# Kernel optimization log

Measured on AMD Instinct MI355X. Metric: run time of the kernel, lower is better.

## Reference

```python
import jax, jax.numpy as jnp
import numpy as np

DIM = 512
CODEBOOK_SIZE = 8192
B, N = 8, 2048
EPS = 1e-12


def setup_inputs() -> dict:
    key = jax.random.key(0)
    k1, k2, k3 = jax.random.split(key, 3)
    x = jax.random.normal(k1, (B, N, DIM), dtype=jnp.float32)
    # matches torch.randn(codebook_size, dim) * dim ** -0.5
    codebook = jax.random.normal(k2, (CODEBOOK_SIZE, DIM), dtype=jnp.float32) * DIM ** -0.5
    # nn.Linear(dim, dim, bias=False) weight, applied as x @ W.T
    W = jax.random.normal(k3, (DIM, DIM), dtype=jnp.float32) * DIM ** -0.5
    return {"x": x, "codebook": codebook, "W": W}


def _l2norm(t):
    return t / jnp.maximum(jnp.linalg.norm(t, axis=-1, keepdims=True), EPS)


def _rotate_from_to(q, x):
    """Rotation trick: forward value == q, gradient flows through x via a
    detached Householder-style rotation (R = I - 2ww^T + 2 q_hat x_hat^T)
    and detached norm rescaling."""
    sg = jax.lax.stop_gradient
    norm_x = jnp.linalg.norm(x, axis=-1, keepdims=True)
    norm_q = jnp.linalg.norm(q, axis=-1, keepdims=True)
    x_hat = x / jnp.maximum(norm_x, EPS)
    q_hat = q / jnp.maximum(norm_q, EPS)
    w = sg(_l2norm(x_hat + q_hat))
    x_hat_d, q_hat_d = sg(x_hat), sg(q_hat)
    e = x
    rotated = (e
               - 2.0 * jnp.sum(e * w, axis=-1, keepdims=True) * w
               + 2.0 * jnp.sum(e * x_hat_d, axis=-1, keepdims=True) * q_hat_d)
    return rotated * sg(norm_q / jnp.maximum(norm_x, EPS))


def reference(x, codebook, W):
    # implicit codebook = Linear(codebook)
    codes = jnp.einsum('cd,ed->ce', codebook, W)  # [C, d]
    d2 = -2.0 * jnp.einsum('bnd,cd->bnc', x, codes) + jnp.sum(codes * codes, axis=-1)
    indices = jnp.argmin(jax.lax.stop_gradient(d2), axis=-1)  # [b, n] int
    quantized = codes[indices]  # gather -> [b, n, d]
    commit_loss = jnp.mean((jax.lax.stop_gradient(x) - quantized) ** 2)
    quantized = _rotate_from_to(quantized, x)
    return quantized, indices, commit_loss
```

## Files before the change

kernel.cpp:

```cpp
#include <hip/hip_runtime.h>


#define DIMK  512
#define CBN   8192
#define MROWS 16384

#define SX 24.0f
#define SC 500.0f
#define INV_SS (1.0f / (SX * SC))
#define DKEY  1231
#define NSLOT 3

#define WS_CODES   0UL
#define WS_XQ      16777216UL
#define WS_CQ      25165824UL
#define WS_NORMS   29360128UL
#define WS_CAND    29392896UL
#define WS_CBH     29392896UL
#define WS_CBL     37781504UL
#define WS_WH      54558720UL
#define WS_WL      55083008UL
#define WS_LOSSP   55607296UL

typedef short s16x8 __attribute__((ext_vector_type(8)));
typedef int   i32x4 __attribute__((ext_vector_type(4)));
typedef float f32x4 __attribute__((ext_vector_type(4)));

__device__ __forceinline__ unsigned short f2bf(float f) {
    unsigned u = __float_as_uint(f);
    unsigned r = u + 0x7FFFu + ((u >> 16) & 1u);
    return (unsigned short)(r >> 16);
}
__device__ __forceinline__ float bf2f(unsigned short h) {
    return __uint_as_float(((unsigned)h) << 16);
}
__device__ __forceinline__ void load_lds16(const void* g, void* l) {
    __builtin_amdgcn_global_load_lds((const __attribute__((address_space(1))) void*)g,
                                     (__attribute__((address_space(3))) void*)l,
                                     16, 0, 0);
}
__device__ __forceinline__ signed char q8(float v, float s) {
    return (signed char)__float2int_rn(fminf(fmaxf(v * s, -127.0f), 127.0f));
}

__global__ __launch_bounds__(256) void prep(
        const float* __restrict__ x, const float* __restrict__ cb, const float* __restrict__ W,
        signed char* __restrict__ xq,
        unsigned short* __restrict__ cbh, unsigned short* __restrict__ cbl,
        unsigned short* __restrict__ wh, unsigned short* __restrict__ wl,
        float* __restrict__ norms) {
    const int b = blockIdx.x;
    const int t = threadIdx.x;
    if (b < 8192) {
        const int i = b * 256 + t;
        float4 v = ((const float4*)x)[i];
        char4 c;
        c.x = q8(v.x, SX); c.y = q8(v.y, SX); c.z = q8(v.z, SX); c.w = q8(v.w, SX);
        ((char4*)xq)[i] = c;
    } else if (b < 12288) {
        const int i = (b - 8192) * 256 + t;
        float4 v = ((const float4*)cb)[i];
        ushort4 h, l;
        h.x = f2bf(v.x); l.x = f2bf(v.x - bf2f(h.x));
        h.y = f2bf(v.y); l.y = f2bf(v.y - bf2f(h.y));
        h.z = f2bf(v.z); l.z = f2bf(v.z - bf2f(h.z));
        h.w = f2bf(v.w); l.w = f2bf(v.w - bf2f(h.w));
        ((ushort4*)cbh)[i] = h;
        ((ushort4*)cbl)[i] = l;
    } else if (b < 12544) {
        const int i = (b - 12288) * 256 + t;
        float4 v = ((const float4*)W)[i];
        ushort4 h, l;
        h.x = f2bf(v.x); l.x = f2bf(v.x - bf2f(h.x));
        h.y = f2bf(v.y); l.y = f2bf(v.y - bf2f(h.y));
        h.z = f2bf(v.z); l.z = f2bf(v.z - bf2f(h.z));
        h.w = f2bf(v.w); l.w = f2bf(v.w - bf2f(h.w));
        ((ushort4*)wh)[i] = h;
        ((ushort4*)wl)[i] = l;
    } else {
        const int i = (b - 12544) * 256 + t;
        norms[i] = 0.0f;
    }
}

__global__ __launch_bounds__(512) void codes_mfma(
        const unsigned short* __restrict__ Ah_g, const unsigned short* __restrict__ Al_g,
        const unsigned short* __restrict__ Bh_g, const unsigned short* __restrict__ Bl_g,
        float* __restrict__ C, signed char* __restrict__ Cq, float* __restrict__ Norms) {
    __shared__ __align__(16) unsigned short Ahi[2][128 * 32];
    __shared__ __align__(16) unsigned short Alo[2][128 * 32];
    __shared__ __align__(16) unsigned short Bhi[2][128 * 32];
    __shared__ __align__(16) unsigned short Blo[2][128 * 32];

    const int t    = threadIdx.x;
    const int w    = t >> 6;
    const int lane = t & 63;
    const int quad = lane >> 4;
    const int l16  = lane & 15;
    const int wm   = w & 3, wn = w >> 2;
    const int rowBase = blockIdx.x * 128;
    const int colBase = blockIdx.y * 128;

    f32x4 acc[2][4];
    #pragma unroll
    for (int i = 0; i < 2; ++i)
        #pragma unroll
        for (int j = 0; j < 4; ++j)
            acc[i][j] = (f32x4)(0.0f);

    const int mr = t >> 2;
    const int kq = ((t & 3) ^ ((t >> 3) & 3)) * 8;
    const size_t gxa = (size_t)(rowBase + mr) * DIMK + kq;
    const size_t gca = (size_t)(colBase + mr) * DIMK + kq;
    const int l0 = w * 512;

    const int swz8 = (quad ^ ((l16 >> 1) & 3)) * 8;

#define CODES_STAGE(NXT, K0)                                   \
    do {                                                       \
        load_lds16(Ah_g + gxa + (K0), &Ahi[NXT][l0]);          \
        load_lds16(Al_g + gxa + (K0), &Alo[NXT][l0]);          \
        load_lds16(Bh_g + gca + (K0), &Bhi[NXT][l0]);          \
        load_lds16(Bl_g + gca + (K0), &Blo[NXT][l0]);          \
    } while (0)

#define CODES_COMPUTE(CUR)                                                                         \
    do {                                                                                           \
        s16x8 ah[2], al[2], bh[4], bl[4];                                                          \
        _Pragma("unroll")                                                                          \
        for (int i = 0; i < 2; ++i) {                                                              \
            const int m = wm * 32 + i * 16 + l16;                                                  \
            ah[i] = *(const s16x8*)&Ahi[CUR][m * 32 + swz8];                                       \
            al[i] = *(const s16x8*)&Alo[CUR][m * 32 + swz8];                                       \
        }                                                                                          \
        _Pragma("unroll")                                                                          \
        for (int j = 0; j < 4; ++j) {                                                              \
            const int n = wn * 64 + j * 16 + l16;                                                  \
            bh[j] = *(const s16x8*)&Bhi[CUR][n * 32 + swz8];                                       \
            bl[j] = *(const s16x8*)&Blo[CUR][n * 32 + swz8];                                       \
        }                                                                                          \
        _Pragma("unroll")                                                                          \
        for (int i = 0; i < 2; ++i)                                                                \
            _Pragma("unroll")                                                                      \
            for (int j = 0; j < 4; ++j) {                                                          \
                acc[i][j] = __builtin_amdgcn_mfma_f32_16x16x32_bf16(ah[i], bh[j], acc[i][j], 0, 0, 0); \
                acc[i][j] = __builtin_amdgcn_mfma_f32_16x16x32_bf16(ah[i], bl[j], acc[i][j], 0, 0, 0); \
                acc[i][j] = __builtin_amdgcn_mfma_f32_16x16x32_bf16(al[i], bh[j], acc[i][j], 0, 0, 0); \
            }                                                                                      \
    } while (0)

    CODES_STAGE(0, 0);
    asm volatile("s_waitcnt vmcnt(0)" ::: "memory");
    __syncthreads();

    for (int k0 = 0; k0 < DIMK; k0 += 64) {
        CODES_STAGE(1, k0 + 32);
        CODES_COMPUTE(0);
        asm volatile("s_waitcnt vmcnt(0)" ::: "memory");
        __syncthreads();
        if (k0 + 64 < DIMK) {
            CODES_STAGE(0, k0 + 64);
            CODES_COMPUTE(1);
            asm volatile("s_waitcnt vmcnt(0)" ::: "memory");
            __syncthreads();
        } else {
            CODES_COMPUTE(1);
        }
    }
#undef CODES_STAGE
#undef CODES_COMPUTE

    #pragma unroll
    for (int i = 0; i < 2; ++i) {
        #pragma unroll
        for (int r = 0; r < 4; ++r) {
            const int row = rowBase + wm * 32 + i * 16 + quad * 4 + r;
            float nsum = 0.0f;
            #pragma unroll
            for (int j = 0; j < 4; ++j) {
                const int col = colBase + wn * 64 + j * 16 + l16;
                const float v = acc[i][j][r];
                C[(size_t)row * DIMK + col] = v;
                Cq[(size_t)row * DIMK + col] = q8(v, SC);
                nsum = fmaf(v, v, nsum);
            }
            nsum += __shfl_xor(nsum, 1, 64);
            nsum += __shfl_xor(nsum, 2, 64);
            nsum += __shfl_xor(nsum, 4, 64);
            nsum += __shfl_xor(nsum, 8, 64);
            if (l16 == 0) atomicAdd(&Norms[row], nsum);
        }
    }
}

__global__ __launch_bounds__(512, 6) void d2_argmin_i8(
        const signed char* __restrict__ Xq,
        const signed char* __restrict__ Cq,
        const float* __restrict__ Norms,
        unsigned* __restrict__ Cand) {
    __shared__ __align__(16) signed char Ash[2][128 * 64];
    __shared__ __align__(16) signed char Bsh[2][128 * 64];

    const int t    = threadIdx.x;
    const int w    = t >> 6;
    const int lane = t & 63;
    const int quad = lane >> 4;
    const int l16  = lane & 15;
    const int wm   = w & 3, wn = w >> 2;
    const int rowBase = blockIdx.x * 128;
    const int colBase = blockIdx.y * 128;

    i32x4 acc[2][4];
    #pragma unroll
    for (int i = 0; i < 2; ++i)
        #pragma unroll
        for (int j = 0; j < 4; ++j)
            acc[i][j] = (i32x4)(0);

    const int mr  = t >> 2;
    const int kcs = ((t & 3) ^ ((t >> 3) & 3)) * 16;
    const size_t gxa = (size_t)(rowBase + mr) * DIMK + kcs;
    const size_t gca = (size_t)(colBase + mr) * DIMK + kcs;
    const int lb = w * 1024;

    const int swz  = (quad ^ ((l16 >> 1) & 3)) * 16;
    const int aoff = (wm * 32 + l16) * 64 + swz;
    const int boff = (wn * 64 + l16) * 64 + swz;

    float nq[4];
    #pragma unroll
    for (int j = 0; j < 4; ++j)
        nq[j] = fmaf(Norms[colBase + wn * 64 + j * 16 + l16], 4096.0f, 65536.0f);

#define D2_STEP(CUR, NXT, K0, DO_STAGE, DO_SYNC)                                                   \
    do {                                                                                           \
        if (DO_STAGE) {                                                                            \
            load_lds16(Xq + gxa + (K0) + 64, &Ash[NXT][lb]);                                       \
            load_lds16(Cq + gca + (K0) + 64, &Bsh[NXT][lb]);                                       \
        }                                                                                          \
        i32x4 af0 = *(const i32x4*)&Ash[CUR][aoff];                                                \
        i32x4 af1 = *(const i32x4*)&Ash[CUR][aoff + 1024];                                         \
        __builtin_amdgcn_s_setprio(1);                                                             \
        _Pragma("unroll")                                                                          \
        for (int j = 0; j < 4; ++j) {                                                              \
            const i32x4 bfj = *(const i32x4*)&Bsh[CUR][boff + j * 1024];                           \
            acc[0][j] = __builtin_amdgcn_mfma_i32_16x16x64_i8(af0, bfj, acc[0][j], 0, 0, 0);       \
            acc[1][j] = __builtin_amdgcn_mfma_i32_16x16x64_i8(af1, bfj, acc[1][j], 0, 0, 0);       \
        }                                                                                          \
        __builtin_amdgcn_s_setprio(0);                                                             \
        if (DO_SYNC) {                                                                             \
            asm volatile("s_waitcnt vmcnt(0)" ::: "memory");                                       \
            __syncthreads();                                                                       \
        }                                                                                          \
    } while (0)

    load_lds16(Xq + gxa, &Ash[0][lb]);
    load_lds16(Cq + gca, &Bsh[0][lb]);
    asm volatile("s_waitcnt vmcnt(0)" ::: "memory");
    __syncthreads();

    D2_STEP(0, 1,   0, true,  true);
    D2_STEP(1, 0,  64, true,  true);
    D2_STEP(0, 1, 128, true,  true);
    D2_STEP(1, 0, 192, true,  true);
    D2_STEP(0, 1, 256, true,  true);
    D2_STEP(1, 0, 320, true,  true);
    D2_STEP(0, 1, 384, true,  true);
    D2_STEP(1, 0, 448, false, false);
#undef D2_STEP

    const unsigned colG = colBase + wn * 64 + l16;
    const int subtile = blockIdx.y * 2 + wn;
    const float C2 = -8192.0f * INV_SS;

    #pragma unroll
    for (int i = 0; i < 2; ++i) {
        #pragma unroll
        for (int r = 0; r < 4; ++r) {
            unsigned k[4];
            #pragma unroll
            for (int j = 0; j < 4; ++j) {
                const float kf = fmaf((float)acc[i][j][r], C2, nq[j]);
                int ki = (int)kf;
                ki = ki < 0 ? 0 : ki;
                ki = ki > 524287 ? 524287 : ki;
                k[j] = ((unsigned)ki << 13) | (colG + j * 16);
            }
            unsigned lo01 = min(k[0], k[1]), hi01 = max(k[0], k[1]);
            unsigned lo23 = min(k[2], k[3]), hi23 = max(k[2], k[3]);
            unsigned a0 = min(lo01, lo23);
            unsigned m  = max(lo01, lo23);
            unsigned tt = min(hi01, hi23);
            unsigned a1 = min(m, tt);
            unsigned a2 = max(m, tt);
            #pragma unroll
            for (int mk = 1; mk < 16; mk <<= 1) {
                const unsigned b0 = __shfl_xor(a0, mk, 64);
                const unsigned b1 = __shfl_xor(a1, mk, 64);
                const unsigned b2 = __shfl_xor(a2, mk, 64);
                const unsigned M0 = max(a0, b0);
                const unsigned m1 = min(a1, b1);
                const unsigned n0 = min(a0, b0);
                a2 = min(max(m1, M0), min(a2, b2));
                a1 = min(M0, m1);
                a0 = n0;
            }
            if (l16 == 0) {
                const int row = rowBase + wm * 32 + i * 16 + quad * 4 + r;
                unsigned* slot = Cand + ((size_t)row * 128 + subtile) * NSLOT;
                slot[0] = a0; slot[1] = a1; slot[2] = a2;
            }
        }
    }
}

__global__ __launch_bounds__(256) void refine_gather(
        const float* __restrict__ X, const float* __restrict__ Codes,
        const float* __restrict__ Norms, const unsigned* __restrict__ Cand,
        float* __restrict__ outQ, float* __restrict__ outIdx,
        float* __restrict__ lossP) {
    const int t    = threadIdx.x;
    const int w    = t >> 6;
    const int lane = t & 63;
    const int row  = blockIdx.x * 4 + w;

    const unsigned* cp = Cand + (size_t)row * 128 * NSLOT + lane * 6;
    unsigned sl[6];
    #pragma unroll
    for (int s = 0; s < 6; ++s) sl[s] = cp[s];

    unsigned mn = sl[0];
    #pragma unroll
    for (int s = 1; s < 6; ++s) mn = min(mn, sl[s]);
    #pragma unroll
    for (int mask = 1; mask < 64; mask <<= 1)
        mn = min(mn, (unsigned)__shfl((int)mn, lane ^ mask, 64));
    const unsigned thrp = (((mn >> 13) + DKEY) << 13) | 0x1FFFu;

    const float4 xa = *(const float4*)(X + (size_t)row * DIMK + lane * 8);
    const float4 xb = *(const float4*)(X + (size_t)row * DIMK + lane * 8 + 4);

    float bestD = __builtin_inff();
    unsigned bestIdx = 0xFFFFFFFFu;

    #pragma unroll
    for (int s = 0; s < 6; ++s) {
        unsigned long long bm = __ballot(sl[s] <= thrp);
        while (bm) {
            const int src = __ffsll(bm) - 1;
            bm &= bm - 1;
            const unsigned sv = (unsigned)__shfl((int)sl[s], src, 64);
            const unsigned idx = sv & 0x1FFFu;
            const float4 ca = *(const float4*)(Codes + (size_t)idx * DIMK + lane * 8);
            const float4 cbv = *(const float4*)(Codes + (size_t)idx * DIMK + lane * 8 + 4);
            float s2 = xa.x * ca.x + xa.y * ca.y + xa.z * ca.z + xa.w * ca.w
                     + xb.x * cbv.x + xb.y * cbv.y + xb.z * cbv.z + xb.w * cbv.w;
            #pragma unroll
            for (int mm = 1; mm < 64; mm <<= 1) s2 += __shfl_xor(s2, mm, 64);
            const float d2 = fmaf(-2.0f, s2, Norms[idx]);
            if (d2 < bestD || (d2 == bestD && idx < bestIdx)) { bestD = d2; bestIdx = idx; }
        }
    }

    const float4 qa = *(const float4*)(Codes + (size_t)bestIdx * DIMK + lane * 8);
    const float4 qb = *(const float4*)(Codes + (size_t)bestIdx * DIMK + lane * 8 + 4);
    *(float4*)(outQ + (size_t)row * DIMK + lane * 8) = qa;
    *(float4*)(outQ + (size_t)row * DIMK + lane * 8 + 4) = qb;
    float dx0 = xa.x - qa.x, dx1 = xa.y - qa.y, dx2 = xa.z - qa.z, dx3 = xa.w - qa.w;
    float dy0 = xb.x - qb.x, dy1 = xb.y - qb.y, dy2 = xb.z - qb.z, dy3 = xb.w - qb.w;
    float s = dx0 * dx0 + dx1 * dx1 + dx2 * dx2 + dx3 * dx3
            + dy0 * dy0 + dy1 * dy1 + dy2 * dy2 + dy3 * dy3;
    #pragma unroll
    for (int off = 32; off > 0; off >>= 1) s += __shfl_down(s, off);
    if (lane == 0) {
        lossP[row] = s;
        outIdx[row] = (float)bestIdx;
    }
}

__global__ __launch_bounds__(1024) void finalize_loss(const float* __restrict__ lossPartials,
                                                      float* __restrict__ outLoss) {
    const int t = threadIdx.x;
    const float4* p = (const float4*)lossPartials;
    const float4 a = p[t];
    const float4 b = p[t + 1024];
    const float4 c = p[t + 2048];
    const float4 d = p[t + 3072];
    float s = (a.x + a.y + a.z + a.w) + (b.x + b.y + b.z + b.w)
            + (c.x + c.y + c.z + c.w) + (d.x + d.y + d.z + d.w);
    #pragma unroll
    for (int off = 32; off > 0; off >>= 1) s += __shfl_down(s, off);
    __shared__ float red[16];
    if ((t & 63) == 0) red[t >> 6] = s;
    __syncthreads();
    if (t < 64) {
        float v = (t < 16) ? red[t] : 0.0f;
        v += __shfl_down(v, 8, 64);
        v += __shfl_down(v, 4, 64);
        v += __shfl_down(v, 2, 64);
        v += __shfl_down(v, 1, 64);
        if (t == 0)
            *outLoss = v * (1.0f / (float)((size_t)MROWS * DIMK));
    }
}

extern "C" void kernel_launch(void* const* d_in, const int* in_sizes, int n_in,
                              void* d_out, int out_size, void* d_ws, size_t ws_size,
                              hipStream_t stream) {
    const float* x  = (const float*)d_in[0];
    const float* cb = (const float*)d_in[1];
    const float* W  = (const float*)d_in[2];
    float* out = (float*)d_out;

    char* ws = (char*)d_ws;
    float* codes          = (float*)(ws + WS_CODES);
    signed char* xq       = (signed char*)(ws + WS_XQ);
    signed char* cq       = (signed char*)(ws + WS_CQ);
    float* norms          = (float*)(ws + WS_NORMS);
    unsigned* cand        = (unsigned*)(ws + WS_CAND);
    unsigned short* cbh   = (unsigned short*)(ws + WS_CBH);
    unsigned short* cbl   = (unsigned short*)(ws + WS_CBL);
    unsigned short* wh    = (unsigned short*)(ws + WS_WH);
    unsigned short* wl    = (unsigned short*)(ws + WS_WL);
    float* lossP          = (float*)(ws + WS_LOSSP);

    prep<<<12576, 256, 0, stream>>>(x, cb, W, xq, cbh, cbl, wh, wl, norms);

    codes_mfma<<<dim3(CBN / 128, DIMK / 128), 512, 0, stream>>>(cbh, cbl, wh, wl, codes, cq, norms);

    d2_argmin_i8<<<dim3(MROWS / 128, CBN / 128), 512, 0, stream>>>(xq, cq, norms, cand);

    refine_gather<<<MROWS / 4, 256, 0, stream>>>(x, codes, norms, cand, out,
                                                 out + (size_t)MROWS * DIMK, lossP);
    finalize_loss<<<1, 1024, 0, stream>>>(lossP, out + (size_t)MROWS * DIMK + MROWS);
}
```

Before: 274.5 us.

## Triple-buffer LDS tiles with partial vmcnt waits in codes and distance GEMMs

Both GEMM kernels move from double to triple-buffered LDS staging. Each step now waits only until the oldest prefetch has landed (partial vmcnt count) and uses a raw s_barrier, so two tiles can be in flight while one is being computed. This is meant to hide global-to-LDS latency that the previous full vmcnt(0) drain exposed. In exchange it uses more LDS per block, which could lower occupancy, and it relies on the raw barrier being enough for ordering between LDS reads and the next overwrite.

```diff
diff --git a/kernel.cpp b/kernel.cpp
--- a/kernel.cpp
+++ b/kernel.cpp
@@ -42,6 +42,13 @@
 __device__ __forceinline__ signed char q8(float v, float s) {
     return (signed char)__float2int_rn(fminf(fmaxf(v * s, -127.0f), 127.0f));
 }
+
+#define WAIT_BAR(N)                                              \
+    do {                                                         \
+        asm volatile("s_waitcnt vmcnt(" #N ")" ::: "memory");    \
+        __builtin_amdgcn_s_barrier();                            \
+        asm volatile("" ::: "memory");                           \
+    } while (0)
 
 __global__ __launch_bounds__(256) void prep(
         const float* __restrict__ x, const float* __restrict__ cb, const float* __restrict__ W,
@@ -87,10 +94,10 @@
         const unsigned short* __restrict__ Ah_g, const unsigned short* __restrict__ Al_g,
         const unsigned short* __restrict__ Bh_g, const unsigned short* __restrict__ Bl_g,
         float* __restrict__ C, signed char* __restrict__ Cq, float* __restrict__ Norms) {
-    __shared__ __align__(16) unsigned short Ahi[2][128 * 32];
-    __shared__ __align__(16) unsigned short Alo[2][128 * 32];
-    __shared__ __align__(16) unsigned short Bhi[2][128 * 32];
-    __shared__ __align__(16) unsigned short Blo[2][128 * 32];
+    __shared__ __align__(16) unsigned short Ahi[3][128 * 32];
+    __shared__ __align__(16) unsigned short Alo[3][128 * 32];
+    __shared__ __align__(16) unsigned short Bhi[3][128 * 32];
+    __shared__ __align__(16) unsigned short Blo[3][128 * 32];
 
     const int t    = threadIdx.x;
     const int w    = t >> 6;
@@ -116,12 +123,12 @@
 
     const int swz8 = (quad ^ ((l16 >> 1) & 3)) * 8;
 
-#define CODES_STAGE(NXT, K0)                                   \
+#define CODES_STAGE(B, K0)                                     \
     do {                                                       \
-        load_lds16(Ah_g + gxa + (K0), &Ahi[NXT][l0]);          \
-        load_lds16(Al_g + gxa + (K0), &Alo[NXT][l0]);          \
-        load_lds16(Bh_g + gca + (K0), &Bhi[NXT][l0]);          \
-        load_lds16(Bl_g + gca + (K0), &Blo[NXT][l0]);          \
+        load_lds16(Ah_g + gxa + (K0), &Ahi[B][l0]);            \
+        load_lds16(Al_g + gxa + (K0), &Alo[B][l0]);            \
+        load_lds16(Bh_g + gca + (K0), &Bhi[B][l0]);            \
+        load_lds16(Bl_g + gca + (K0), &Blo[B][l0]);            \
     } while (0)
 
 #define CODES_COMPUTE(CUR)                                                                         \
@@ -150,23 +157,25 @@
     } while (0)
 
     CODES_STAGE(0, 0);
-    asm volatile("s_waitcnt vmcnt(0)" ::: "memory");
-    __syncthreads();
-
-    for (int k0 = 0; k0 < DIMK; k0 += 64) {
-        CODES_STAGE(1, k0 + 32);
-        CODES_COMPUTE(0);
-        asm volatile("s_waitcnt vmcnt(0)" ::: "memory");
-        __syncthreads();
-        if (k0 + 64 < DIMK) {
-            CODES_STAGE(0, k0 + 64);
-            CODES_COMPUTE(1);
-            asm volatile("s_waitcnt vmcnt(0)" ::: "memory");
-            __syncthreads();
-        } else {
-            CODES_COMPUTE(1);
-        }
-    }
+    CODES_STAGE(1, 32);
+    WAIT_BAR(4);
+
+    CODES_STAGE(2,  64); CODES_COMPUTE(0); WAIT_BAR(4);
+    CODES_STAGE(0,  96); CODES_COMPUTE(1); WAIT_BAR(4);
+    CODES_STAGE(1, 128); CODES_COMPUTE(2); WAIT_BAR(4);
+    CODES_STAGE(2, 160); CODES_COMPUTE(0); WAIT_BAR(4);
+    CODES_STAGE(0, 192); CODES_COMPUTE(1); WAIT_BAR(4);
+    CODES_STAGE(1, 224); CODES_COMPUTE(2); WAIT_BAR(4);
+    CODES_STAGE(2, 256); CODES_COMPUTE(0); WAIT_BAR(4);
+    CODES_STAGE(0, 288); CODES_COMPUTE(1); WAIT_BAR(4);
+    CODES_STAGE(1, 320); CODES_COMPUTE(2); WAIT_BAR(4);
+    CODES_STAGE(2, 352); CODES_COMPUTE(0); WAIT_BAR(4);
+    CODES_STAGE(0, 384); CODES_COMPUTE(1); WAIT_BAR(4);
+    CODES_STAGE(1, 416); CODES_COMPUTE(2); WAIT_BAR(4);
+    CODES_STAGE(2, 448); CODES_COMPUTE(0); WAIT_BAR(4);
+    CODES_STAGE(0, 480); CODES_COMPUTE(1); WAIT_BAR(4);
+    CODES_COMPUTE(2);                   WAIT_BAR(0);
+    CODES_COMPUTE(0);
 #undef CODES_STAGE
 #undef CODES_COMPUTE
 
@@ -198,8 +207,8 @@
         const signed char* __restrict__ Cq,
         const float* __restrict__ Norms,
         unsigned* __restrict__ Cand) {
-    __shared__ __align__(16) signed char Ash[2][128 * 64];
-    __shared__ __align__(16) signed char Bsh[2][128 * 64];
+    __shared__ __align__(16) signed char Ash[3][128 * 64];
+    __shared__ __align__(16) signed char Bsh[3][128 * 64];
 
     const int t    = threadIdx.x;
     const int w    = t >> 6;
@@ -232,12 +241,14 @@
     for (int j = 0; j < 4; ++j)
         nq[j] = fmaf(Norms[colBase + wn * 64 + j * 16 + l16], 4096.0f, 65536.0f);
 
-#define D2_STEP(CUR, NXT, K0, DO_STAGE, DO_SYNC)                                                   \
+#define D2_STAGE(B, K0)                                        \
+    do {                                                       \
+        load_lds16(Xq + gxa + (K0), &Ash[B][lb]);              \
+        load_lds16(Cq + gca + (K0), &Bsh[B][lb]);              \
+    } while (0)
+
+#define D2_COMPUTE(CUR)                                                                            \
     do {                                                                                           \
-        if (DO_STAGE) {                                                                            \
-            load_lds16(Xq + gxa + (K0) + 64, &Ash[NXT][lb]);                                       \
-            load_lds16(Cq + gca + (K0) + 64, &Bsh[NXT][lb]);                                       \
-        }                                                                                          \
         i32x4 af0 = *(const i32x4*)&Ash[CUR][aoff];                                                \
         i32x4 af1 = *(const i32x4*)&Ash[CUR][aoff + 1024];                                         \
         __builtin_amdgcn_s_setprio(1);                                                             \
@@ -248,26 +259,22 @@
             acc[1][j] = __builtin_amdgcn_mfma_i32_16x16x64_i8(af1, bfj, acc[1][j], 0, 0, 0);       \
         }                                                                                          \
         __builtin_amdgcn_s_setprio(0);                                                             \
-        if (DO_SYNC) {                                                                             \
-            asm volatile("s_waitcnt vmcnt(0)" ::: "memory");                                       \
-            __syncthreads();                                                                       \
-        }                                                                                          \
     } while (0)
 
-    load_lds16(Xq + gxa, &Ash[0][lb]);
-    load_lds16(Cq + gca, &Bsh[0][lb]);
-    asm volatile("s_waitcnt vmcnt(0)" ::: "memory");
-    __syncthreads();
-
-    D2_STEP(0, 1,   0, true,  true);
-    D2_STEP(1, 0,  64, true,  true);
-    D2_STEP(0, 1, 128, true,  true);
-    D2_STEP(1, 0, 192, true,  true);
-    D2_STEP(0, 1, 256, true,  true);
-    D2_STEP(1, 0, 320, true,  true);
-    D2_STEP(0, 1, 384, true,  true);
-    D2_STEP(1, 0, 448, false, false);
-#undef D2_STEP
+    D2_STAGE(0, 0);
+    D2_STAGE(1, 64);
+    WAIT_BAR(2);
+
+    D2_STAGE(2, 128); D2_COMPUTE(0); WAIT_BAR(2);
+    D2_STAGE(0, 192); D2_COMPUTE(1); WAIT_BAR(2);
+    D2_STAGE(1, 256); D2_COMPUTE(2); WAIT_BAR(2);
+    D2_STAGE(2, 320); D2_COMPUTE(0); WAIT_BAR(2);
+    D2_STAGE(0, 384); D2_COMPUTE(1); WAIT_BAR(2);
+    D2_STAGE(1, 448); D2_COMPUTE(2); WAIT_BAR(2);
+    D2_COMPUTE(0);                   WAIT_BAR(0);
+    D2_COMPUTE(1);
+#undef D2_STAGE
+#undef D2_COMPUTE
 
     const unsigned colG = colBase + wn * 64 + l16;
     const int subtile = blockIdx.y * 2 + wn;
```

New measurement: 278.7 us. No clear change (+1.5%).
